# Kernel tuning notes

Measured on AMD Instinct MI355X. Metric: run time of the kernel, lower is better.

## Reference

```python
import jax, jax.numpy as jnp
import numpy as np

RES = 7          # POOLER_RESOLUTION
SR = 2           # POOLER_SAMPLING_RATIO
SCALES = (0.25, 0.125, 0.0625, 0.03125)
CANONICAL_SCALE = 224.0
CANONICAL_LEVEL = 4.0
K_MIN, K_MAX = 2.0, 5.0  # -log2(SCALES[0]), -log2(SCALES[-1])


def setup_inputs() -> dict:
    key = jax.random.key(0)
    ks = jax.random.split(key, 9)
    feat0 = jax.random.normal(ks[0], (2, 256, 200, 200), dtype=jnp.float32)
    feat1 = jax.random.normal(ks[1], (2, 256, 100, 100), dtype=jnp.float32)
    feat2 = jax.random.normal(ks[2], (2, 256, 50, 50), dtype=jnp.float32)
    feat3 = jax.random.normal(ks[3], (2, 256, 25, 25), dtype=jnp.float32)
    R = 512
    x1 = jax.random.uniform(ks[4], (R,)) * 600.0
    y1 = jax.random.uniform(ks[5], (R,)) * 600.0
    w = 16.0 + jax.random.uniform(ks[6], (R,)) * 500.0
    h = 16.0 + jax.random.uniform(ks[7], (R,)) * 500.0
    boxes = jnp.stack([x1, y1, x1 + w, y1 + h], axis=1).astype(jnp.float32)
    batch_idx = jax.random.randint(ks[8], (R,), 0, 2, dtype=jnp.int32)
    return {"feat0": feat0, "feat1": feat1, "feat2": feat2, "feat3": feat3,
            "boxes": boxes, "batch_idx": batch_idx}


def _map_levels(boxes):
    # LevelMapper: floor(k0 + log2(sqrt(area)/224 + eps)), clamp to [k_min,k_max], shift
    area = jnp.maximum(boxes[:, 2] - boxes[:, 0], 0.0) * jnp.maximum(boxes[:, 3] - boxes[:, 1], 0.0)
    s = jnp.sqrt(area)
    lvl = jnp.floor(CANONICAL_LEVEL + jnp.log2(s / CANONICAL_SCALE + 1e-6))
    return (jnp.clip(lvl, K_MIN, K_MAX) - K_MIN).astype(jnp.int32)


def _roi_align(feat, boxes, batch_idx, scale):
    # feat: [B,C,H,W]; boxes: [R,4] (x1,y1,x2,y2) in image coords; ROIAlign (aligned=False)
    H, W = feat.shape[2], feat.shape[3]
    x1 = boxes[:, 0] * scale
    y1 = boxes[:, 1] * scale
    x2 = boxes[:, 2] * scale
    y2 = boxes[:, 3] * scale
    roi_w = jnp.maximum(x2 - x1, 1.0)
    roi_h = jnp.maximum(y2 - y1, 1.0)
    bin_w = roi_w / RES
    bin_h = roi_h / RES
    # sample-point offsets within the roi, in bin units: [RES*SR]
    p = (jnp.arange(RES, dtype=jnp.float32)[:, None]
         + (jnp.arange(SR, dtype=jnp.float32)[None, :] + 0.5) / SR).reshape(-1)
    ys = y1[:, None] + p[None, :] * bin_h[:, None]   # [R,S]
    xs = x1[:, None] + p[None, :] * bin_w[:, None]   # [R,S]
    valid_y = (ys >= -1.0) & (ys <= float(H))
    valid_x = (xs >= -1.0) & (xs <= float(W))
    yc = jnp.clip(ys, 0.0, float(H - 1))
    xc = jnp.clip(xs, 0.0, float(W - 1))
    y0 = jnp.floor(yc).astype(jnp.int32)
    x0 = jnp.floor(xc).astype(jnp.int32)
    y1i = jnp.minimum(y0 + 1, H - 1)
    x1i = jnp.minimum(x0 + 1, W - 1)
    ly = yc - y0.astype(jnp.float32)
    lx = xc - x0.astype(jnp.float32)
    hy = 1.0 - ly
    hx = 1.0 - lx
    b = batch_idx[:, None, None]  # [R,1,1]

    def gather(yi, xi):
        # advanced indexing -> [R,S,S,C]
        return feat[b, :, yi[:, :, None], xi[:, None, :]]

    v = (gather(y0, x0) * (hy[:, :, None] * hx[:, None, :])[..., None]
         + gather(y0, x1i) * (hy[:, :, None] * lx[:, None, :])[..., None]
         + gather(y1i, x0) * (ly[:, :, None] * hx[:, None, :])[..., None]
         + gather(y1i, x1i) * (ly[:, :, None] * lx[:, None, :])[..., None])
    v = v * (valid_y[:, :, None] & valid_x[:, None, :])[..., None].astype(v.dtype)
    R = boxes.shape[0]
    C = feat.shape[1]
    v = v.reshape(R, RES, SR, RES, SR, C).mean(axis=(2, 4))  # [R,RES,RES,C]
    return jnp.transpose(v, (0, 3, 1, 2))  # [R,C,RES,RES]


def reference(feat0, feat1, feat2, feat3, boxes, batch_idx):
    feats = (feat0, feat1, feat2, feat3)
    levels = _map_levels(boxes)
    out = jnp.zeros((boxes.shape[0], feat0.shape[1], RES, RES), dtype=feat0.dtype)
    for lvl, (f, sc) in enumerate(zip(feats, SCALES)):
        pooled = _roi_align(f, boxes, batch_idx, sc)
        out = out + jnp.where((levels == lvl)[:, None, None, None], pooled, 0.0)
    return out
```

## Files before the change

### kernel.cpp

```cpp
#include <hip/hip_runtime.h>
#include <hip/hip_bf16.h>

#define RES 7
#define NCH 256

__device__ __forceinline__ unsigned short f32_to_bf16_rne(float f) {
    unsigned int u = __float_as_uint(f);
    u += 0x7fffu + ((u >> 16) & 1u);
    return (unsigned short)(u >> 16);
}

__device__ __forceinline__ unsigned int pack_bf16x2(float lo, float hi) {
    return (unsigned int)f32_to_bf16_rne(lo) | ((unsigned int)f32_to_bf16_rne(hi) << 16);
}

__global__ __launch_bounds__(512) void transpose_all_bf16_v4(
    const float* __restrict__ f0, const float* __restrict__ f1,
    const float* __restrict__ f2, const float* __restrict__ f3,
    unsigned short* __restrict__ ws)
{
    __shared__ unsigned short lds[256 * 68];

    const int xt = blockIdx.x;
    const int cy = blockIdx.y;
    const int b  = blockIdx.z;

    const int l    = (xt >= 157) + (xt >= 197) + (xt >= 207);
    const int base = (l == 0) ? 0 : (l == 1) ? 157 : (l == 2) ? 197 : 207;
    const int HW   = (l == 0) ? 40000 : (l == 1) ? 10000 : (l == 2) ? 2500 : 625;
    const float* __restrict__ src =
        (l == 0) ? f0 : (l == 1) ? f1 : (l == 2) ? f2 : f3;
    const size_t doff = (l == 0) ? 0u : (l == 1) ? 20480000u
                      : (l == 2) ? 25600000u : 26880000u;

    const int hw0 = (xt - base) * 256;
    const int c0b = 64 * cy;

    const float* __restrict__ s    = src + (size_t)b * NCH * HW;
    unsigned short* __restrict__ d = ws + doff + (size_t)b * HW * NCH;

    const int t   = threadIdx.x;
    const int hq  = t & 63;
    const int cg  = t >> 6;
    const int hwq = hw0 + 4 * hq;

#pragma unroll
    for (int sweep = 0; sweep < 2; ++sweep) {
        const int cl = 4 * (cg + 8 * sweep);
        const int c0 = c0b + cl;
        float va[4][4];
        if (hwq + 3 < HW) {
#pragma unroll
            for (int i = 0; i < 4; ++i) {
                const float4 f = *(const float4*)(s + (size_t)(c0 + i) * HW + hwq);
                va[i][0] = f.x; va[i][1] = f.y; va[i][2] = f.z; va[i][3] = f.w;
            }
        } else {
#pragma unroll
            for (int i = 0; i < 4; ++i)
#pragma unroll
                for (int j = 0; j < 4; ++j)
                    va[i][j] = (hwq + j < HW) ? s[(size_t)(c0 + i) * HW + hwq + j] : 0.0f;
        }
#pragma unroll
        for (int j = 0; j < 4; ++j) {
            uint2 p;
            p.x = pack_bf16x2(va[0][j], va[1][j]);
            p.y = pack_bf16x2(va[2][j], va[3][j]);
            *(uint2*)&lds[(4 * hq + j) * 68 + cl] = p;
        }
    }
    __syncthreads();

#pragma unroll
    for (int j = 0; j < 8; ++j) {
        const int idx = t + 512 * j;
        const int row = idx >> 4;
        const int u   = idx & 15;
        const int hw  = hw0 + row;
        if (hw < HW) {
            const uint2 p = *(const uint2*)&lds[row * 68 + 4 * u];
            *(uint2*)(d + (size_t)hw * NCH + c0b + 4 * u) = p;
        }
    }
}

__global__ __launch_bounds__(512) void roi_gather_nhwc_bf16(
    const unsigned short* __restrict__ ws,
    const float* __restrict__ boxes, const int* __restrict__ bidx,
    float* __restrict__ out)
{
    __shared__ float lds[49 * 260];

    const int r   = blockIdx.x;
    const int t   = threadIdx.x;
    const int cq  = t & 63;
    const int grp = t >> 6;

    const float bx1 = boxes[r * 4 + 0];
    const float by1 = boxes[r * 4 + 1];
    const float bx2 = boxes[r * 4 + 2];
    const float by2 = boxes[r * 4 + 3];

    const float area = fmaxf(bx2 - bx1, 0.0f) * fmaxf(by2 - by1, 0.0f);
    const float s    = sqrtf(area);
    const float lvlf = floorf(4.0f + log2f(s / 224.0f + 1e-6f));
    const int   lvl  = (int)(fminf(fmaxf(lvlf, 2.0f), 5.0f)) - 2;

    float scale; int H; size_t off;
    if      (lvl == 0) { scale = 0.25f;    H = 200; off = 0u; }
    else if (lvl == 1) { scale = 0.125f;   H = 100; off = 20480000u; }
    else if (lvl == 2) { scale = 0.0625f;  H = 50;  off = 25600000u; }
    else               { scale = 0.03125f; H = 25;  off = 26880000u; }
    const int W = H;

    const int b = bidx[r];
    const unsigned short* __restrict__ feat = ws + off + (size_t)b * H * W * NCH;

    const float x1 = bx1 * scale;
    const float y1 = by1 * scale;
    const float roi_w = fmaxf(bx2 * scale - x1, 1.0f);
    const float roi_h = fmaxf(by2 * scale - y1, 1.0f);
    const float bw = roi_w * (1.0f / RES);
    const float bh = roi_h * (1.0f / RES);

    for (int bin = grp; bin < 49; bin += 8) {
        const int py = bin / 7;
        const int px = bin - py * 7;

        float acc0 = 0.0f, acc1 = 0.0f, acc2 = 0.0f, acc3 = 0.0f;
#pragma unroll
        for (int sy = 0; sy < 2; ++sy) {
            const float pyf = (float)py + ((float)sy + 0.5f) * 0.5f;
            const float ysmp = y1 + pyf * bh;
            const bool  vy   = (ysmp >= -1.0f) && (ysmp <= (float)H);
            const float ycl  = fminf(fmaxf(ysmp, 0.0f), (float)(H - 1));
            const int   y0   = (int)floorf(ycl);
            const int   y1i  = min(y0 + 1, H - 1);
            const float ly   = ycl - (float)y0;
            const float hy   = 1.0f - ly;
#pragma unroll
            for (int sx = 0; sx < 2; ++sx) {
                const float pxf = (float)px + ((float)sx + 0.5f) * 0.5f;
                const float xsmp = x1 + pxf * bw;
                const bool  vx   = (xsmp >= -1.0f) && (xsmp <= (float)W);
                const float xcl  = fminf(fmaxf(xsmp, 0.0f), (float)(W - 1));
                const int   x0   = (int)floorf(xcl);
                const int   x1i  = min(x0 + 1, W - 1);
                const float lx   = xcl - (float)x0;
                const float hx   = 1.0f - lx;

                const float m   = (vy && vx) ? 1.0f : 0.0f;
                const float w00 = m * hy * hx;
                const float w01 = m * hy * lx;
                const float w10 = m * ly * hx;
                const float w11 = m * ly * lx;

                const uint2 u00 = *(const uint2*)(feat + ((size_t)(y0  * W + x0 )) * NCH + 4 * cq);
                const uint2 u01 = *(const uint2*)(feat + ((size_t)(y0  * W + x1i)) * NCH + 4 * cq);
                const uint2 u10 = *(const uint2*)(feat + ((size_t)(y1i * W + x0 )) * NCH + 4 * cq);
                const uint2 u11 = *(const uint2*)(feat + ((size_t)(y1i * W + x1i)) * NCH + 4 * cq);

                acc0 += w00 * __uint_as_float(u00.x << 16)
                      + w01 * __uint_as_float(u01.x << 16)
                      + w10 * __uint_as_float(u10.x << 16)
                      + w11 * __uint_as_float(u11.x << 16);
                acc1 += w00 * __uint_as_float(u00.x & 0xffff0000u)
                      + w01 * __uint_as_float(u01.x & 0xffff0000u)
                      + w10 * __uint_as_float(u10.x & 0xffff0000u)
                      + w11 * __uint_as_float(u11.x & 0xffff0000u);
                acc2 += w00 * __uint_as_float(u00.y << 16)
                      + w01 * __uint_as_float(u01.y << 16)
                      + w10 * __uint_as_float(u10.y << 16)
                      + w11 * __uint_as_float(u11.y << 16);
                acc3 += w00 * __uint_as_float(u00.y & 0xffff0000u)
                      + w01 * __uint_as_float(u01.y & 0xffff0000u)
                      + w10 * __uint_as_float(u10.y & 0xffff0000u)
                      + w11 * __uint_as_float(u11.y & 0xffff0000u);
            }
        }
        float4* dst = (float4*)&lds[bin * 260 + 4 * cq];
        *dst = make_float4(acc0 * 0.25f, acc1 * 0.25f, acc2 * 0.25f, acc3 * 0.25f);
    }

    __syncthreads();

    float* __restrict__ o = out + (size_t)r * (NCH * 49);
    for (int i = t; i < NCH * 49; i += 512) {
        const int ch = i / 49;
        const int bn = i - ch * 49;
        o[i] = lds[bn * 260 + ch];
    }
}

__global__ __launch_bounds__(256) void roi_align_fpn_kernel(
    const float* __restrict__ f0, const float* __restrict__ f1,
    const float* __restrict__ f2, const float* __restrict__ f3,
    const float* __restrict__ boxes, const int* __restrict__ bidx,
    float* __restrict__ out)
{
    const int r   = blockIdx.x;
    const int bin = blockIdx.y;
    const int c   = threadIdx.x;
    const int py  = bin / RES;
    const int px  = bin - py * RES;

    const float bx1 = boxes[r * 4 + 0];
    const float by1 = boxes[r * 4 + 1];
    const float bx2 = boxes[r * 4 + 2];
    const float by2 = boxes[r * 4 + 3];

    const float area = fmaxf(bx2 - bx1, 0.0f) * fmaxf(by2 - by1, 0.0f);
    const float s    = sqrtf(area);
    const float lvlf = floorf(4.0f + log2f(s / 224.0f + 1e-6f));
    const int   lvl  = (int)(fminf(fmaxf(lvlf, 2.0f), 5.0f)) - 2;

    const float scales[4] = {0.25f, 0.125f, 0.0625f, 0.03125f};
    const int   Hs[4]     = {200, 100, 50, 25};
    const float* feats[4] = {f0, f1, f2, f3};

    const float scale = scales[lvl];
    const int   H     = Hs[lvl];
    const int   W     = H;
    const float* feat = feats[lvl];

    const int b = bidx[r];

    const float x1 = bx1 * scale;
    const float y1 = by1 * scale;
    const float roi_w = fmaxf(bx2 * scale - x1, 1.0f);
    const float roi_h = fmaxf(by2 * scale - y1, 1.0f);
    const float bw = roi_w * (1.0f / RES);
    const float bh = roi_h * (1.0f / RES);

    const float* __restrict__ fc = feat + (size_t)(b * NCH + c) * H * W;

    float acc = 0.0f;
#pragma unroll
    for (int sy = 0; sy < 2; ++sy) {
        const float pyf = (float)py + ((float)sy + 0.5f) * 0.5f;
        const float ys  = y1 + pyf * bh;
        const bool  vy  = (ys >= -1.0f) && (ys <= (float)H);
        const float ycl = fminf(fmaxf(ys, 0.0f), (float)(H - 1));
        const int   y0  = (int)floorf(ycl);
        const int   y1i = min(y0 + 1, H - 1);
        const float ly  = ycl - (float)y0;
        const float hy  = 1.0f - ly;
#pragma unroll
        for (int sx = 0; sx < 2; ++sx) {
            const float pxf = (float)px + ((float)sx + 0.5f) * 0.5f;
            const float xs  = x1 + pxf * bw;
            const bool  vx  = (xs >= -1.0f) && (xs <= (float)W);
            const float xcl = fminf(fmaxf(xs, 0.0f), (float)(W - 1));
            const int   x0  = (int)floorf(xcl);
            const int   x1i = min(x0 + 1, W - 1);
            const float lx  = xcl - (float)x0;
            const float hx  = 1.0f - lx;

            const float v00 = fc[y0  * W + x0 ];
            const float v01 = fc[y0  * W + x1i];
            const float v10 = fc[y1i * W + x0 ];
            const float v11 = fc[y1i * W + x1i];

            const float v = v00 * (hy * hx) + v01 * (hy * lx)
                          + v10 * (ly * hx) + v11 * (ly * lx);
            if (vy && vx) acc += v;
        }
    }

    out[((size_t)r * NCH + c) * (RES * RES) + bin] = acc * 0.25f;
}

extern "C" void kernel_launch(void* const* d_in, const int* in_sizes, int n_in,
                              void* d_out, int out_size, void* d_ws, size_t ws_size,
                              hipStream_t stream)
{
    const float* f0    = (const float*)d_in[0];
    const float* f1    = (const float*)d_in[1];
    const float* f2    = (const float*)d_in[2];
    const float* f3    = (const float*)d_in[3];
    const float* boxes = (const float*)d_in[4];
    const int*   bidx  = (const int*)d_in[5];
    float* out = (float*)d_out;

    const int R = in_sizes[4] / 4;

    const size_t need = 27200000ull * sizeof(unsigned short);

    if (ws_size >= need) {
        unsigned short* ws = (unsigned short*)d_ws;
        transpose_all_bf16_v4<<<dim3(210, 4, 2), dim3(512), 0, stream>>>(f0, f1, f2, f3, ws);
        roi_gather_nhwc_bf16<<<dim3(R), dim3(512), 0, stream>>>(ws, boxes, bidx, out);
    } else {
        dim3 grid(R, RES * RES);
        roi_align_fpn_kernel<<<grid, dim3(NCH), 0, stream>>>(f0, f1, f2, f3, boxes, bidx, out);
    }
}
```

Before: 49.43 us.

## Make feature transpose persistent with atomic work-stealing over smaller tiles

Replaces the fixed 3D grid of transpose blocks with 1024 persistent blocks. They pull 128-position by 64-channel tile jobs from a global atomic counter stored in the workspace; a grid-stride fallback is used when the workspace is too small for the counter. The goal is better load balance across CUs and less tail imbalance between pyramid levels of very different sizes. In exchange it adds a memset launch to reset the counter, an atomic and an extra barrier per job, and smaller tiles that each amortise less.

After: 85.16 us. +72.3%, slower.

```diff
diff --git a/kernel.cpp b/kernel.cpp
--- a/kernel.cpp
+++ b/kernel.cpp
@@ -3,6 +3,13 @@
 
 #define RES 7
 #define NCH 256
+
+#define WS_BF16_ELEMS 27200000ull
+#define CTR_OFFSET_BYTES 54400000ull
+
+#define NJOBS 3336
+#define JOBS_PER_BATCH 1668
+#define JOBS_PER_CG 417
 
 __device__ __forceinline__ unsigned short f32_to_bf16_rne(float f) {
     unsigned int u = __float_as_uint(f);
@@ -14,40 +21,45 @@
     return (unsigned int)f32_to_bf16_rne(lo) | ((unsigned int)f32_to_bf16_rne(hi) << 16);
 }
 
-__global__ __launch_bounds__(512) void transpose_all_bf16_v4(
+__global__ __launch_bounds__(512) void transpose_ws_bf16(
     const float* __restrict__ f0, const float* __restrict__ f1,
     const float* __restrict__ f2, const float* __restrict__ f3,
-    unsigned short* __restrict__ ws)
-{
-    __shared__ unsigned short lds[256 * 68];
-
-    const int xt = blockIdx.x;
-    const int cy = blockIdx.y;
-    const int b  = blockIdx.z;
-
-    const int l    = (xt >= 157) + (xt >= 197) + (xt >= 207);
-    const int base = (l == 0) ? 0 : (l == 1) ? 157 : (l == 2) ? 197 : 207;
-    const int HW   = (l == 0) ? 40000 : (l == 1) ? 10000 : (l == 2) ? 2500 : 625;
-    const float* __restrict__ src =
-        (l == 0) ? f0 : (l == 1) ? f1 : (l == 2) ? f2 : f3;
-    const size_t doff = (l == 0) ? 0u : (l == 1) ? 20480000u
-                      : (l == 2) ? 25600000u : 26880000u;
-
-    const int hw0 = (xt - base) * 256;
-    const int c0b = 64 * cy;
-
-    const float* __restrict__ s    = src + (size_t)b * NCH * HW;
-    unsigned short* __restrict__ d = ws + doff + (size_t)b * HW * NCH;
-
-    const int t   = threadIdx.x;
-    const int hq  = t & 63;
-    const int cg  = t >> 6;
-    const int hwq = hw0 + 4 * hq;
-
-#pragma unroll
-    for (int sweep = 0; sweep < 2; ++sweep) {
-        const int cl = 4 * (cg + 8 * sweep);
-        const int c0 = c0b + cl;
+    unsigned short* __restrict__ ws, unsigned int* __restrict__ counter)
+{
+    __shared__ unsigned short lds[128 * 68];
+    __shared__ int job_s;
+
+    const int t  = threadIdx.x;
+    const int hq = t & 31;
+    const int cr = t >> 5;
+
+    for (;;) {
+        if (t == 0) job_s = (int)atomicAdd(counter, 1u);
+        __syncthreads();
+        const int j = job_s;
+        if (j >= NJOBS) break;
+
+        const int b   = (j >= JOBS_PER_BATCH) ? 1 : 0;
+        const int rem = j - b * JOBS_PER_BATCH;
+        const int cg  = rem / JOBS_PER_CG;
+        const int xt  = rem - cg * JOBS_PER_CG;
+
+        const int l    = (xt >= 313) + (xt >= 392) + (xt >= 412);
+        const int base = (l == 0) ? 0 : (l == 1) ? 313 : (l == 2) ? 392 : 412;
+        const int HW   = (l == 0) ? 40000 : (l == 1) ? 10000 : (l == 2) ? 2500 : 625;
+        const float* __restrict__ src =
+            (l == 0) ? f0 : (l == 1) ? f1 : (l == 2) ? f2 : f3;
+        const size_t doff = (l == 0) ? 0u : (l == 1) ? 20480000u
+                          : (l == 2) ? 25600000u : 26880000u;
+
+        const int hw0 = (xt - base) * 128;
+        const int c0b = 64 * cg;
+        const int c0  = c0b + 4 * cr;
+        const int hwq = hw0 + 4 * hq;
+
+        const float* __restrict__ s    = src + (size_t)b * NCH * HW;
+        unsigned short* __restrict__ d = ws + doff + (size_t)b * HW * NCH;
+
         float va[4][4];
         if (hwq + 3 < HW) {
 #pragma unroll
@@ -59,28 +71,28 @@
 #pragma unroll
             for (int i = 0; i < 4; ++i)
 #pragma unroll
-                for (int j = 0; j < 4; ++j)
-                    va[i][j] = (hwq + j < HW) ? s[(size_t)(c0 + i) * HW + hwq + j] : 0.0f;
-        }
-#pragma unroll
-        for (int j = 0; j < 4; ++j) {
+                for (int jj = 0; jj < 4; ++jj)
+                    va[i][jj] = (hwq + jj < HW) ? s[(size_t)(c0 + i) * HW + hwq + jj] : 0.0f;
+        }
+#pragma unroll
+        for (int jj = 0; jj < 4; ++jj) {
             uint2 p;
-            p.x = pack_bf16x2(va[0][j], va[1][j]);
-            p.y = pack_bf16x2(va[2][j], va[3][j]);
-            *(uint2*)&lds[(4 * hq + j) * 68 + cl] = p;
-        }
-    }
-    __syncthreads();
-
-#pragma unroll
-    for (int j = 0; j < 8; ++j) {
-        const int idx = t + 512 * j;
-        const int row = idx >> 4;
-        const int u   = idx & 15;
-        const int hw  = hw0 + row;
-        if (hw < HW) {
-            const uint2 p = *(const uint2*)&lds[row * 68 + 4 * u];
-            *(uint2*)(d + (size_t)hw * NCH + c0b + 4 * u) = p;
+            p.x = pack_bf16x2(va[0][jj], va[1][jj]);
+            p.y = pack_bf16x2(va[2][jj], va[3][jj]);
+            *(uint2*)&lds[(4 * hq + jj) * 68 + 4 * cr] = p;
+        }
+        __syncthreads();
+
+#pragma unroll
+        for (int it = 0; it < 4; ++it) {
+            const int idx = t + 512 * it;
+            const int row = idx >> 4;
+            const int u   = idx & 15;
+            const int hw  = hw0 + row;
+            if (hw < HW) {
+                const uint2 p = *(const uint2*)&lds[row * 68 + 4 * u];
+                *(uint2*)(d + (size_t)hw * NCH + c0b + 4 * u) = p;
+            }
         }
     }
 }
@@ -193,6 +205,75 @@
     }
 }
 
+__global__ __launch_bounds__(512) void transpose_fixed_bf16(
+    const float* __restrict__ f0, const float* __restrict__ f1,
+    const float* __restrict__ f2, const float* __restrict__ f3,
+    unsigned short* __restrict__ ws)
+{
+    __shared__ unsigned short lds[128 * 68];
+    const int t  = threadIdx.x;
+    const int hq = t & 31;
+    const int cr = t >> 5;
+
+    for (int j = blockIdx.x; j < NJOBS; j += gridDim.x) {
+        const int b   = (j >= JOBS_PER_BATCH) ? 1 : 0;
+        const int rem = j - b * JOBS_PER_BATCH;
+        const int cg  = rem / JOBS_PER_CG;
+        const int xt  = rem - cg * JOBS_PER_CG;
+
+        const int l    = (xt >= 313) + (xt >= 392) + (xt >= 412);
+        const int base = (l == 0) ? 0 : (l == 1) ? 313 : (l == 2) ? 392 : 412;
+        const int HW   = (l == 0) ? 40000 : (l == 1) ? 10000 : (l == 2) ? 2500 : 625;
+        const float* __restrict__ src =
+            (l == 0) ? f0 : (l == 1) ? f1 : (l == 2) ? f2 : f3;
+        const size_t doff = (l == 0) ? 0u : (l == 1) ? 20480000u
+                          : (l == 2) ? 25600000u : 26880000u;
+
+        const int hw0 = (xt - base) * 128;
+        const int c0b = 64 * cg;
+        const int c0  = c0b + 4 * cr;
+        const int hwq = hw0 + 4 * hq;
+
+        const float* __restrict__ s    = src + (size_t)b * NCH * HW;
+        unsigned short* __restrict__ d = ws + doff + (size_t)b * HW * NCH;
+
+        float va[4][4];
+        if (hwq + 3 < HW) {
+#pragma unroll
+            for (int i = 0; i < 4; ++i) {
+                const float4 f = *(const float4*)(s + (size_t)(c0 + i) * HW + hwq);
+                va[i][0] = f.x; va[i][1] = f.y; va[i][2] = f.z; va[i][3] = f.w;
+            }
+        } else {
+#pragma unroll
+            for (int i = 0; i < 4; ++i)
+#pragma unroll
+                for (int jj = 0; jj < 4; ++jj)
+                    va[i][jj] = (hwq + jj < HW) ? s[(size_t)(c0 + i) * HW + hwq + jj] : 0.0f;
+        }
+#pragma unroll
+        for (int jj = 0; jj < 4; ++jj) {
+            uint2 p;
+            p.x = pack_bf16x2(va[0][jj], va[1][jj]);
+            p.y = pack_bf16x2(va[2][jj], va[3][jj]);
+            *(uint2*)&lds[(4 * hq + jj) * 68 + 4 * cr] = p;
+        }
+        __syncthreads();
+#pragma unroll
+        for (int it = 0; it < 4; ++it) {
+            const int idx = t + 512 * it;
+            const int row = idx >> 4;
+            const int u   = idx & 15;
+            const int hw  = hw0 + row;
+            if (hw < HW) {
+                const uint2 p = *(const uint2*)&lds[row * 68 + 4 * u];
+                *(uint2*)(d + (size_t)hw * NCH + c0b + 4 * u) = p;
+            }
+        }
+        __syncthreads();
+    }
+}
+
 __global__ __launch_bounds__(256) void roi_align_fpn_kernel(
     const float* __restrict__ f0, const float* __restrict__ f1,
     const float* __restrict__ f2, const float* __restrict__ f3,
@@ -285,11 +366,20 @@
 
     const int R = in_sizes[4] / 4;
 
-    const size_t need = 27200000ull * sizeof(unsigned short);
-
-    if (ws_size >= need) {
+    const size_t need_ws  = WS_BF16_ELEMS * sizeof(unsigned short);
+    const size_t need_ctr = CTR_OFFSET_BYTES + sizeof(unsigned int);
+
+    if (ws_size >= need_ws) {
         unsigned short* ws = (unsigned short*)d_ws;
-        transpose_all_bf16_v4<<<dim3(210, 4, 2), dim3(512), 0, stream>>>(f0, f1, f2, f3, ws);
+        if (ws_size >= need_ctr) {
+            unsigned int* counter = (unsigned int*)((char*)d_ws + CTR_OFFSET_BYTES);
+            hipMemsetAsync(counter, 0, sizeof(unsigned int), stream);
+            transpose_ws_bf16<<<dim3(1024), dim3(512), 0, stream>>>(
+                f0, f1, f2, f3, ws, counter);
+        } else {
+            transpose_fixed_bf16<<<dim3(1024), dim3(512), 0, stream>>>(
+                f0, f1, f2, f3, ws);
+        }
         roi_gather_nhwc_bf16<<<dim3(R), dim3(512), 0, stream>>>(ws, boxes, bidx, out);
     } else {
         dim3 grid(R, RES * RES);
```

## Use direct global-to-LDS loads in NCHW-to-NHWC bf16 transpose

Applied to the files above, without the earlier changes.

Rewrites the feature-map transpose to load fp32 rows straight into LDS with global_load_lds, skipping the trip through registers, and halves the spatial tile to 128 so the grid has twice as many blocks. The bf16 packing moves from the load phase to the store phase, where values are read back from LDS as fp32. Tail tiles and maps whose size is not a multiple of 4 fall back to scalar loads. This costs more LDS traffic per element and relies on the LDS layout the DMA path produces, which could cause bank conflicts on the strided readback.

New measurement: 51.01 us. +3.2%, slower.

```diff
diff --git a/kernel.cpp b/kernel.cpp
--- a/kernel.cpp
+++ b/kernel.cpp
@@ -14,72 +14,84 @@
     return (unsigned int)f32_to_bf16_rne(lo) | ((unsigned int)f32_to_bf16_rne(hi) << 16);
 }
 
-__global__ __launch_bounds__(512) void transpose_all_bf16_v4(
+__global__ __launch_bounds__(512) void transpose_dma_bf16(
     const float* __restrict__ f0, const float* __restrict__ f1,
     const float* __restrict__ f2, const float* __restrict__ f3,
     unsigned short* __restrict__ ws)
 {
-    __shared__ unsigned short lds[256 * 68];
+    __shared__ float ldsf[32 * 260];
 
     const int xt = blockIdx.x;
     const int cy = blockIdx.y;
     const int b  = blockIdx.z;
 
-    const int l    = (xt >= 157) + (xt >= 197) + (xt >= 207);
-    const int base = (l == 0) ? 0 : (l == 1) ? 157 : (l == 2) ? 197 : 207;
+    const int l    = (xt >= 313) + (xt >= 392) + (xt >= 412);
+    const int base = (l == 0) ? 0 : (l == 1) ? 313 : (l == 2) ? 392 : 412;
     const int HW   = (l == 0) ? 40000 : (l == 1) ? 10000 : (l == 2) ? 2500 : 625;
     const float* __restrict__ src =
         (l == 0) ? f0 : (l == 1) ? f1 : (l == 2) ? f2 : f3;
     const size_t doff = (l == 0) ? 0u : (l == 1) ? 20480000u
                       : (l == 2) ? 25600000u : 26880000u;
 
-    const int hw0 = (xt - base) * 256;
+    const int hw0 = (xt - base) * 128;
     const int c0b = 64 * cy;
 
     const float* __restrict__ s    = src + (size_t)b * NCH * HW;
     unsigned short* __restrict__ d = ws + doff + (size_t)b * HW * NCH;
 
-    const int t   = threadIdx.x;
-    const int hq  = t & 63;
-    const int cg  = t >> 6;
-    const int hwq = hw0 + 4 * hq;
-
-#pragma unroll
-    for (int sweep = 0; sweep < 2; ++sweep) {
-        const int cl = 4 * (cg + 8 * sweep);
-        const int c0 = c0b + cl;
+    const int t  = threadIdx.x;
+    const int w  = t >> 6;
+    const int ln = t & 63;
+
+    const bool dma = (hw0 + 128 <= HW) && ((HW & 3) == 0);
+
+    if (dma) {
+#pragma unroll
+        for (int q = 0; q < 4; ++q) {
+            const int g = w * 4 + q;
+            const int c = c0b + 2 * g + (ln >> 5);
+            const float* gp = s + (size_t)c * HW + hw0 + (ln & 31) * 4;
+            float* lp = &ldsf[g * 260];
+            __builtin_amdgcn_global_load_lds(
+                (const __attribute__((address_space(1))) void*)gp,
+                (__attribute__((address_space(3))) void*)lp,
+                16, 0, 0);
+        }
+    } else {
+        const int hq  = t & 31;
+        const int cr  = t >> 5;
+        const int hwq = hw0 + 4 * hq;
         float va[4][4];
-        if (hwq + 3 < HW) {
-#pragma unroll
-            for (int i = 0; i < 4; ++i) {
-                const float4 f = *(const float4*)(s + (size_t)(c0 + i) * HW + hwq);
-                va[i][0] = f.x; va[i][1] = f.y; va[i][2] = f.z; va[i][3] = f.w;
-            }
-        } else {
-#pragma unroll
-            for (int i = 0; i < 4; ++i)
-#pragma unroll
-                for (int j = 0; j < 4; ++j)
-                    va[i][j] = (hwq + j < HW) ? s[(size_t)(c0 + i) * HW + hwq + j] : 0.0f;
-        }
-#pragma unroll
-        for (int j = 0; j < 4; ++j) {
-            uint2 p;
-            p.x = pack_bf16x2(va[0][j], va[1][j]);
-            p.y = pack_bf16x2(va[2][j], va[3][j]);
-            *(uint2*)&lds[(4 * hq + j) * 68 + cl] = p;
+#pragma unroll
+        for (int i = 0; i < 4; ++i)
+#pragma unroll
+            for (int j = 0; j < 4; ++j)
+                va[i][j] = (hwq + j < HW)
+                         ? s[(size_t)(c0b + 4 * cr + i) * HW + hwq + j] : 0.0f;
+#pragma unroll
+        for (int i = 0; i < 4; ++i) {
+            const int c = 4 * cr + i;
+#pragma unroll
+            for (int j = 0; j < 4; ++j)
+                ldsf[(c >> 1) * 260 + (c & 1) * 128 + 4 * hq + j] = va[i][j];
         }
     }
     __syncthreads();
 
 #pragma unroll
-    for (int j = 0; j < 8; ++j) {
-        const int idx = t + 512 * j;
+    for (int it = 0; it < 4; ++it) {
+        const int idx = t + 512 * it;
         const int row = idx >> 4;
         const int u   = idx & 15;
         const int hw  = hw0 + row;
         if (hw < HW) {
-            const uint2 p = *(const uint2*)&lds[row * 68 + 4 * u];
+            const float v0 = ldsf[(2 * u) * 260 + row];
+            const float v1 = ldsf[(2 * u) * 260 + 128 + row];
+            const float v2 = ldsf[(2 * u + 1) * 260 + row];
+            const float v3 = ldsf[(2 * u + 1) * 260 + 128 + row];
+            uint2 p;
+            p.x = pack_bf16x2(v0, v1);
+            p.y = pack_bf16x2(v2, v3);
             *(uint2*)(d + (size_t)hw * NCH + c0b + 4 * u) = p;
         }
     }
@@ -289,7 +301,7 @@
 
     if (ws_size >= need) {
         unsigned short* ws = (unsigned short*)d_ws;
-        transpose_all_bf16_v4<<<dim3(210, 4, 2), dim3(512), 0, stream>>>(f0, f1, f2, f3, ws);
+        transpose_dma_bf16<<<dim3(417, 4, 2), dim3(512), 0, stream>>>(f0, f1, f2, f3, ws);
         roi_gather_nhwc_bf16<<<dim3(R), dim3(512), 0, stream>>>(ws, boxes, bidx, out);
     } else {
         dim3 grid(R, RES * RES);
```
